# Kernel optimization log

Hardware: AMD Instinct MI355X
Metric: run time of the kernel (lower is better)

The kernel has to match this reference:

```python
import jax, jax.numpy as jnp
import numpy as np

E = 1024      # embed_dim
H = 16        # num_heads
D = E // H    # head_dim
F = 4096      # ff_dim
EPS = 1e-5


def setup_inputs() -> dict:
    key = jax.random.key(0)
    ks = jax.random.split(key, 12)
    s = 0.02
    return {
        "x": jax.random.normal(ks[0], (2, 2048, E), dtype=jnp.float32),
        "qkv_w": jax.random.normal(ks[1], (3 * E, E), dtype=jnp.float32) * s,
        "qkv_b": jnp.zeros((3 * E,), dtype=jnp.float32),
        "out_w": jax.random.normal(ks[2], (E, E), dtype=jnp.float32) * s,
        "out_b": jnp.zeros((E,), dtype=jnp.float32),
        "ff1_w": jax.random.normal(ks[3], (F, E), dtype=jnp.float32) * s,
        "ff1_b": jnp.zeros((F,), dtype=jnp.float32),
        "ff2_w": jax.random.normal(ks[4], (E, F), dtype=jnp.float32) * s,
        "ff2_b": jnp.zeros((E,), dtype=jnp.float32),
        "ln1_g": jnp.ones((E,), dtype=jnp.float32),
        "ln1_b": jnp.zeros((E,), dtype=jnp.float32),
        "ln2_g": jnp.ones((E,), dtype=jnp.float32),
        "ln2_b": jnp.zeros((E,), dtype=jnp.float32),
    }


def _layernorm(x, g, b):
    mu = jnp.mean(x, axis=-1, keepdims=True)
    var = jnp.mean(jnp.square(x - mu), axis=-1, keepdims=True)
    return (x - mu) * jax.lax.rsqrt(var + EPS) * g + b


def reference(x, qkv_w, qkv_b, out_w, out_b, ff1_w, ff1_b, ff2_w, ff2_b,
              ln1_g, ln1_b, ln2_g, ln2_b):
    B, S, _ = x.shape
    scale = D ** -0.5

    # --- attention sublayer (pre-LN) ---
    h = _layernorm(x, ln1_g, ln1_b)
    qkv = h @ qkv_w.T + qkv_b                          # [B,S,3E]
    qkv = qkv.reshape(B, S, 3, H, D)
    q, k, v = qkv[:, :, 0], qkv[:, :, 1], qkv[:, :, 2]  # [B,S,H,D]
    scores = jnp.einsum("bqhd,bkhd->bhqk", q, k) * scale
    attn = jax.nn.softmax(scores, axis=-1)
    o = jnp.einsum("bhqk,bkhd->bqhd", attn, v).reshape(B, S, E)
    x = x + o @ out_w.T + out_b

    # --- FFN sublayer (pre-LN, exact GELU) ---
    h = _layernorm(x, ln2_g, ln2_b)
    h = jax.nn.gelu(h @ ff1_w.T + ff1_b, approximate=False)
    x = x + h @ ff2_w.T + ff2_b
    return x
```

## Files before the change

### kernel.cpp

```cpp
#include <hip/hip_runtime.h>
#include <math.h>


typedef __attribute__((ext_vector_type(8))) short short8;
typedef __attribute__((ext_vector_type(4))) float f32x4;

__device__ __forceinline__ unsigned short f2bf(float f) {
  unsigned int u = __float_as_uint(f);
  u += 0x7fffu + ((u >> 16) & 1u);
  return (unsigned short)(u >> 16);
}

__device__ __forceinline__ float fexp2(float x) {
  return __builtin_amdgcn_exp2f(x);
}

__device__ __forceinline__ short8 pack8(float4 a, float4 b) {
  short8 p;
  p[0] = (short)f2bf(a.x); p[1] = (short)f2bf(a.y);
  p[2] = (short)f2bf(a.z); p[3] = (short)f2bf(a.w);
  p[4] = (short)f2bf(b.x); p[5] = (short)f2bf(b.y);
  p[6] = (short)f2bf(b.z); p[7] = (short)f2bf(b.w);
  return p;
}

__device__ __forceinline__ float gelu_fast(float v) {
  float g = 0.7978845608f * fmaf(0.044715f * v, v * v, v);
  float den = 1.0f + fexp2(-2.885390082f * g);
  return v * __builtin_amdgcn_rcpf(den);
}

__device__ __forceinline__ void async16(const void* g, void* l) {
  __builtin_amdgcn_global_load_lds(
      (const __attribute__((address_space(1))) unsigned int*)g,
      (__attribute__((address_space(3))) unsigned int*)l, 16, 0, 0);
}

__global__ __launch_bounds__(256) void conv_all(
    const float* __restrict__ i0, unsigned short* __restrict__ o0, int n0,
    const float* __restrict__ i1, unsigned short* __restrict__ o1, int n1,
    const float* __restrict__ i2, unsigned short* __restrict__ o2, int n2,
    const float* __restrict__ i3, unsigned short* __restrict__ o3, int n3) {
  int i = blockIdx.x * 256 + threadIdx.x;
  const float* in; unsigned short* out;
  if (i < n0) { in = i0; out = o0; }
  else if ((i -= n0) < n1) { in = i1; out = o1; }
  else if ((i -= n1) < n2) { in = i2; out = o2; }
  else { i -= n2; in = i3; out = o3; if (i >= n3) return; }
  float4 v = ((const float4*)in)[i];
  ushort4 u;
  u.x = f2bf(v.x); u.y = f2bf(v.y); u.z = f2bf(v.z); u.w = f2bf(v.w);
  ((ushort4*)out)[i] = u;
}

__global__ __launch_bounds__(256) void ln_kernel(const float* __restrict__ x,
                                                 const float* __restrict__ g,
                                                 const float* __restrict__ b,
                                                 unsigned short* __restrict__ out) {
  int row = blockIdx.x;
  int t = threadIdx.x;
  const float4* x4 = (const float4*)(x + (size_t)row * 1024);
  float4 v = x4[t];
  float s1 = v.x + v.y + v.z + v.w;
  float s2 = v.x * v.x + v.y * v.y + v.z * v.z + v.w * v.w;
  for (int off = 1; off < 64; off <<= 1) {
    s1 += __shfl_xor(s1, off, 64);
    s2 += __shfl_xor(s2, off, 64);
  }
  __shared__ float r1[4], r2[4];
  int w = t >> 6, lane = t & 63;
  if (lane == 0) { r1[w] = s1; r2[w] = s2; }
  __syncthreads();
  s1 = r1[0] + r1[1] + r1[2] + r1[3];
  s2 = r2[0] + r2[1] + r2[2] + r2[3];
  float mu = s1 * (1.0f / 1024.0f);
  float var = s2 * (1.0f / 1024.0f) - mu * mu;
  float rstd = rsqrtf(var + 1e-5f);
  int c = t * 4;
  float4 gv = ((const float4*)g)[t];
  float4 bv = ((const float4*)b)[t];
  unsigned short* o = out + (size_t)row * 1024 + c;
  o[0] = f2bf((v.x - mu) * rstd * gv.x + bv.x);
  o[1] = f2bf((v.y - mu) * rstd * gv.y + bv.y);
  o[2] = f2bf((v.z - mu) * rstd * gv.z + bv.z);
  o[3] = f2bf((v.w - mu) * rstd * gv.w + bv.w);
}

template <int MODE, int BM, int BN, int BK, int LIN, int NW, int WROWS>
__global__ __launch_bounds__(NW * 64) void gemm_bt(
    const unsigned short* __restrict__ A, const unsigned short* __restrict__ W,
    const float* __restrict__ bias, int M, int N, int K,
    const float* __restrict__ resid, float* __restrict__ out_f32,
    unsigned short* __restrict__ out_bf16,
    unsigned short* __restrict__ qbp, unsigned short* __restrict__ kbp,
    unsigned short* __restrict__ vtb) {
  constexpr int WCOLS = NW / WROWS;
  constexpr int WSPAN = BM / WROWS;
  constexpr int MI = WSPAN / 16;
  constexpr int CW = BN / WCOLS;
  constexpr int NJ = CW / 16;
  constexpr int LPR = BK / 8;
  constexpr int RPW = 512 / BK;
  constexpr int RRND = NW * RPW;
  constexpr int NIA = BM / RRND;
  constexpr int NIW = BN / RRND;
  constexpr int KK = BK / 32;
  static_assert(MODE != 0 || (NW == 4 && BN == 128 && WROWS == 2),
                "MODE 0 epilogue assumes NW=4/BN=128/WROWS=2");
  static_assert(MODE != 2 || CW == 64, "MODE 2 pack path assumes CW=64");
  __shared__ __attribute__((aligned(16))) unsigned short As[2][BM * BK];
  __shared__ __attribute__((aligned(16))) unsigned short Ws[2][BN * BK];
  int tid = threadIdx.x;
  int w = tid >> 6, lane = tid & 63, quad = lane >> 4, l16 = lane & 15;
  int wrow = w / WCOLS, wcol = w % WCOLS;
  int m0, n0;
  if (LIN) {
    int id = blockIdx.x;
    int mc = M / BM;
    m0 = (id % mc) * BM;
    n0 = (id / mc) * BN;
  } else {
    m0 = blockIdx.y * BM;
    n0 = blockIdx.x * BN;
  }

  int srow = lane / LPR;
  int sseg = lane % LPR;
  int ssw = (BK == 64) ? (srow & 7) : ((srow >> 1) & 3);
  int scol = (sseg ^ ssw) * 8;
  const unsigned short* Ag = A + (size_t)(m0 + w * RPW + srow) * K + scol;
  const unsigned short* Wg = W + (size_t)(n0 + w * RPW + srow) * K + scol;

  f32x4 acc[MI][NJ] = {};

#pragma unroll
  for (int i = 0; i < NIA; i++)
    async16(Ag + (size_t)(i * RRND) * K, As[0] + (i * RRND + w * RPW) * BK);
#pragma unroll
  for (int i = 0; i < NIW; i++)
    async16(Wg + (size_t)(i * RRND) * K, Ws[0] + (i * RRND + w * RPW) * BK);

  int fsw = (BK == 64) ? (l16 & 7) : ((l16 >> 1) & 3);

  for (int k0 = 0; k0 < K; k0 += BK) {
    int buf = (k0 / BK) & 1;
    __syncthreads();
    if (k0 + BK < K) {
      int nb = buf ^ 1;
#pragma unroll
      for (int i = 0; i < NIA; i++)
        async16(Ag + (size_t)(i * RRND) * K + k0 + BK, As[nb] + (i * RRND + w * RPW) * BK);
#pragma unroll
      for (int i = 0; i < NIW; i++)
        async16(Wg + (size_t)(i * RRND) * K + k0 + BK, Ws[nb] + (i * RRND + w * RPW) * BK);
    }
    if constexpr (MI >= 8) {
#pragma unroll
      for (int kk = 0; kk < KK; kk++) {
        short8 bfr[NJ];
#pragma unroll
        for (int j = 0; j < NJ; j++)
          bfr[j] = *(const short8*)(Ws[buf] + (wcol * CW + j * 16 + l16) * BK +
                                    ((kk * 4 + quad) ^ fsw) * 8);
#pragma unroll
        for (int i = 0; i < MI; i++) {
          short8 afr = *(const short8*)(As[buf] + (wrow * WSPAN + i * 16 + l16) * BK +
                                        ((kk * 4 + quad) ^ fsw) * 8);
#pragma unroll
          for (int j = 0; j < NJ; j++)
            acc[i][j] = __builtin_amdgcn_mfma_f32_16x16x32_bf16(afr, bfr[j], acc[i][j], 0, 0, 0);
        }
      }
    } else {
      short8 af[MI][KK], bf[NJ][KK];
#pragma unroll
      for (int i = 0; i < MI; i++)
#pragma unroll
        for (int kk = 0; kk < KK; kk++)
          af[i][kk] = *(const short8*)(As[buf] + (wrow * WSPAN + i * 16 + l16) * BK +
                                       ((kk * 4 + quad) ^ fsw) * 8);
#pragma unroll
      for (int j = 0; j < NJ; j++)
#pragma unroll
        for (int kk = 0; kk < KK; kk++)
          bf[j][kk] = *(const short8*)(Ws[buf] + (wcol * CW + j * 16 + l16) * BK +
                                       ((kk * 4 + quad) ^ fsw) * 8);
#pragma unroll
      for (int kk = 0; kk < KK; kk++)
#pragma unroll
        for (int i = 0; i < MI; i++)
#pragma unroll
          for (int j = 0; j < NJ; j++)
            acc[i][j] = __builtin_amdgcn_mfma_f32_16x16x32_bf16(af[i][kk], bf[j][kk], acc[i][j], 0, 0, 0);
    }
  }

  __syncthreads();
  constexpr int EPF = 16 * CW;
  float* ep = (w < NW / 2) ? ((float*)As + w * EPF)
                           : ((float*)Ws + (w - NW / 2) * EPF);
  int orow = lane >> 2;
  int oseg = lane & 3;
  int colbase = n0 + wcol * CW;
  float bv[NJ];
#pragma unroll
  for (int j = 0; j < NJ; j++) bv[j] = bias[colbase + j * 16 + l16];

  if (MODE == 1 || MODE == 2) {
#pragma unroll
    for (int i = 0; i < MI; i++) {
#pragma unroll
      for (int j = 0; j < NJ; j++)
#pragma unroll
        for (int r = 0; r < 4; r++) {
          int row = quad * 4 + r, col = j * 16 + l16;
          float v = acc[i][j][r] + bv[j];
          if (MODE == 2) v = gelu_fast(v);
          ep[row * CW + (((col >> 2) ^ (row & 7)) << 2) + (col & 3)] = v;
        }
      asm volatile("s_waitcnt lgkmcnt(0)" ::: "memory");
      int grow = m0 + wrow * WSPAN + i * 16 + orow;
      if (MODE == 1) {
#pragma unroll
        for (int t = 0; t < CW / 16; t++) {
          int sl = t * 4 + oseg;
          float4 v = *(float4*)(ep + orow * CW + ((sl ^ (orow & 7)) << 2));
          const float4 rv = *(const float4*)(resid + (size_t)grow * N + colbase + sl * 4);
          v.x += rv.x; v.y += rv.y; v.z += rv.z; v.w += rv.w;
          *(float4*)(out_f32 + (size_t)grow * N + colbase + sl * 4) = v;
        }
      } else {
#pragma unroll
        for (int t = 0; t < 2; t++) {
          int s0 = t * 8 + oseg * 2;
          float4 a = *(float4*)(ep + orow * 64 + ((s0 ^ (orow & 7)) << 2));
          float4 b = *(float4*)(ep + orow * 64 + (((s0 + 1) ^ (orow & 7)) << 2));
          *(short8*)(out_bf16 + (size_t)grow * N + colbase + t * 32 + oseg * 8) = pack8(a, b);
        }
      }
      asm volatile("s_waitcnt lgkmcnt(0)" ::: "memory");
    }
  } else {
    int whichW = colbase >> 10;
    int hh = (colbase & 1023) >> 6;
    int bh = (m0 >> 11) * 16 + hh;
    int sbase = (m0 & 2047) + wrow * WSPAN;
    if (whichW < 2) {
      unsigned short* dst0 = (whichW == 0) ? qbp : kbp;
      float qs = (whichW == 0) ? 0.1803368801f : 1.0f;
#pragma unroll
      for (int i = 0; i < MI; i++) {
#pragma unroll
        for (int j = 0; j < NJ; j++)
#pragma unroll
          for (int r = 0; r < 4; r++) {
            int row = quad * 4 + r, col = j * 16 + l16;
            ep[row * 64 + (((col >> 2) ^ (row & 7)) << 2) + (col & 3)] =
                (acc[i][j][r] + bv[j]) * qs;
          }
        asm volatile("s_waitcnt lgkmcnt(0)" ::: "memory");
        int s = sbase + i * 16 + orow;
#pragma unroll
        for (int t = 0; t < 2; t++) {
          int s0 = t * 8 + oseg * 2;
          float4 a = *(float4*)(ep + orow * 64 + ((s0 ^ (orow & 7)) << 2));
          float4 b = *(float4*)(ep + orow * 64 + (((s0 + 1) ^ (orow & 7)) << 2));
          *(short8*)(dst0 + ((size_t)bh * 2048 + s) * 64 + t * 32 + oseg * 8) = pack8(a, b);
        }
        asm volatile("s_waitcnt lgkmcnt(0)" ::: "memory");
      }
    } else {
#pragma unroll
      for (int j = 0; j < NJ; j++) {
#pragma unroll
        for (int i = 0; i < MI; i++) {
          float4 v4;
          v4.x = acc[i][j][0] + bv[j];
          v4.y = acc[i][j][1] + bv[j];
          v4.z = acc[i][j][2] + bv[j];
          v4.w = acc[i][j][3] + bv[j];
          *(float4*)(ep + l16 * 64 + (((i * 4 + quad) ^ (l16 & 7)) << 2)) = v4;
        }
        asm volatile("s_waitcnt lgkmcnt(0)" ::: "memory");
        int d = j * 16 + orow;
#pragma unroll
        for (int t = 0; t < 2; t++) {
          int s0 = t * 8 + oseg * 2;
          float4 a = *(float4*)(ep + orow * 64 + ((s0 ^ (orow & 7)) << 2));
          float4 b = *(float4*)(ep + orow * 64 + (((s0 + 1) ^ (orow & 7)) << 2));
          *(short8*)(vtb + ((size_t)bh * 64 + d) * 2048 + sbase + t * 32 + oseg * 8) = pack8(a, b);
        }
        asm volatile("s_waitcnt lgkmcnt(0)" ::: "memory");
      }
    }
  }
}

#define ALDP 72

__global__ __launch_bounds__(512) void attn_kernel(const unsigned short* __restrict__ qb,
                                                   const unsigned short* __restrict__ kb,
                                                   const unsigned short* __restrict__ vtb,
                                                   unsigned short* __restrict__ ob) {
  __shared__ __attribute__((aligned(16))) unsigned short Ks[2][64 * 64];
  __shared__ __attribute__((aligned(16))) unsigned short Vs[2][64 * 64];
  __shared__ __attribute__((aligned(16))) unsigned short Ps[8][16 * ALDP];

  int tid = threadIdx.x;
  int w = tid >> 6, lane = tid & 63, quad = lane >> 4, l16 = lane & 15;
  int bi = blockIdx.x;
  int bh = (bi & 7) * 4 + ((bi >> 3) & 3);
  int q0 = (bi >> 5) * 128 + w * 16;

  const unsigned short* qbase = qb + ((size_t)bh * 2048 + q0) * 64;
  const unsigned short* kbase = kb + (size_t)bh * 2048 * 64;
  const unsigned short* vbase = vtb + (size_t)bh * 64 * 2048;
  unsigned short* Pw = Ps[w];

  int srow = lane >> 3;
  int scol = ((lane & 7) ^ srow) * 8;
  const unsigned short* kg0 = kbase + (size_t)(w * 8 + srow) * 64 + scol;
  const unsigned short* vg0 = vbase + (size_t)(w * 8 + srow) * 2048 + scol;

  short8 qf[2];
  qf[0] = *(const short8*)(qbase + l16 * 64 + quad * 8);
  qf[1] = *(const short8*)(qbase + l16 * 64 + 32 + quad * 8);

  float lsum = 0.0f;
  f32x4 oacc[4] = {};
  int sw = l16 & 7;

  async16(kg0, &Ks[0][(w * 8) * 64]);
  async16(vg0, &Vs[0][(w * 8) * 64]);

  for (int c0 = 0; c0 < 2048; c0 += 64) {
    int buf = (c0 >> 6) & 1;
    __syncthreads();
    if (c0 + 64 < 2048) {
      int nb = buf ^ 1;
      async16(kg0 + (size_t)(c0 + 64) * 64, &Ks[nb][(w * 8) * 64]);
      async16(vg0 + c0 + 64, &Vs[nb][(w * 8) * 64]);
    }
    short8 kf[4][2];
#pragma unroll
    for (int t = 0; t < 4; t++) {
      const unsigned short* kr = &Ks[buf][(t * 16 + l16) * 64];
      kf[t][0] = *(const short8*)(kr + (quad ^ sw) * 8);
      kf[t][1] = *(const short8*)(kr + ((4 + quad) ^ sw) * 8);
    }
    f32x4 s[4];
#pragma unroll
    for (int t = 0; t < 4; t++) {
      f32x4 z = {0.0f, 0.0f, 0.0f, 0.0f};
      z = __builtin_amdgcn_mfma_f32_16x16x32_bf16(kf[t][0], qf[0], z, 0, 0, 0);
      z = __builtin_amdgcn_mfma_f32_16x16x32_bf16(kf[t][1], qf[1], z, 0, 0, 0);
      s[t] = z;
    }
    float rsum = 0.0f;
    unsigned short* pr = Pw + l16 * ALDP;
#pragma unroll
    for (int t = 0; t < 4; t++) {
      float p0 = fexp2(s[t][0]);
      float p1 = fexp2(s[t][1]);
      float p2 = fexp2(s[t][2]);
      float p3 = fexp2(s[t][3]);
      rsum += (p0 + p1) + (p2 + p3);
      uint2 pk;
      pk.x = __builtin_amdgcn_perm(__float_as_uint(p1), __float_as_uint(p0), 0x07060302u);
      pk.y = __builtin_amdgcn_perm(__float_as_uint(p3), __float_as_uint(p2), 0x07060302u);
      *(uint2*)(pr + t * 16 + quad * 4) = pk;
    }
    rsum += __shfl_xor(rsum, 16, 64);
    rsum += __shfl_xor(rsum, 32, 64);
    lsum += rsum;
    asm volatile("s_waitcnt lgkmcnt(0)" ::: "memory");
#pragma unroll
    for (int ks = 0; ks < 2; ks++) {
      short8 af = *(const short8*)(Pw + l16 * ALDP + ks * 32 + quad * 8);
#pragma unroll
      for (int j = 0; j < 4; j++) {
        short8 vf = *(const short8*)(&Vs[buf][(j * 16 + l16) * 64] +
                                     ((ks * 4 + quad) ^ sw) * 8);
        oacc[j] = __builtin_amdgcn_mfma_f32_16x16x32_bf16(af, vf, oacc[j], 0, 0, 0);
      }
    }
  }

  float linv[4];
#pragma unroll
  for (int r = 0; r < 4; r++)
    linv[r] = __builtin_amdgcn_rcpf(__shfl(lsum, quad * 4 + r, 64));
  int bb = bh >> 4, hh = bh & 15;
#pragma unroll
  for (int j = 0; j < 4; j++)
#pragma unroll
    for (int r = 0; r < 4; r++) {
      size_t tok = (size_t)bb * 2048 + q0 + quad * 4 + r;
      ob[tok * 1024 + hh * 64 + j * 16 + l16] = f2bf(oacc[j][r] * linv[r]);
    }
}

extern "C" void kernel_launch(void* const* d_in, const int* in_sizes, int n_in,
                              void* d_out, int out_size, void* d_ws, size_t ws_size,
                              hipStream_t stream) {
  (void)in_sizes; (void)n_in; (void)out_size; (void)ws_size;
  const float* x     = (const float*)d_in[0];
  const float* qkv_w = (const float*)d_in[1];
  const float* qkv_b = (const float*)d_in[2];
  const float* out_w = (const float*)d_in[3];
  const float* out_b = (const float*)d_in[4];
  const float* ff1_w = (const float*)d_in[5];
  const float* ff1_b = (const float*)d_in[6];
  const float* ff2_w = (const float*)d_in[7];
  const float* ff2_b = (const float*)d_in[8];
  const float* ln1_g = (const float*)d_in[9];
  const float* ln1_b = (const float*)d_in[10];
  const float* ln2_g = (const float*)d_in[11];
  const float* ln2_b = (const float*)d_in[12];
  float* out = (float*)d_out;
  char* ws = (char*)d_ws;

  const int M = 4096;

  unsigned short* WQ = (unsigned short*)(ws + 0);
  unsigned short* WO = (unsigned short*)(ws + 6291456);
  unsigned short* W1 = (unsigned short*)(ws + 8388608);
  unsigned short* W2 = (unsigned short*)(ws + 16777216);
  unsigned short* Hb = (unsigned short*)(ws + 25165824);
  unsigned short* Qb = (unsigned short*)(ws + 33554432);
  unsigned short* Kb = (unsigned short*)(ws + 41943040);
  unsigned short* VT = (unsigned short*)(ws + 50331648);
  unsigned short* Ob = (unsigned short*)(ws + 58720256);
  float*          X1 = (float*)(ws + 67108864);
  unsigned short* Gb = (unsigned short*)(ws + 33554432);

  conv_all<<<12288, 256, 0, stream>>>(qkv_w, WQ, 786432, out_w, WO, 262144,
                                      ff1_w, W1, 1048576, ff2_w, W2, 1048576);

  ln_kernel<<<4096, 256, 0, stream>>>(x, ln1_g, ln1_b, Hb);

  gemm_bt<0, 128, 128, 32, 0, 4, 2><<<dim3(24, 32), 256, 0, stream>>>(
      Hb, WQ, qkv_b, M, 3072, 1024, nullptr, nullptr, nullptr, Qb, Kb, VT);

  attn_kernel<<<512, 512, 0, stream>>>(Qb, Kb, VT, Ob);

  gemm_bt<1, 64, 128, 64, 1, 8, 2><<<512, 512, 0, stream>>>(
      Ob, WO, out_b, M, 1024, 1024, x, X1, nullptr, nullptr, nullptr, nullptr);

  ln_kernel<<<4096, 256, 0, stream>>>(X1, ln2_g, ln2_b, Hb);

  gemm_bt<2, 256, 256, 64, 0, 8, 2><<<dim3(16, 16), 512, 0, stream>>>(
      Hb, W1, ff1_b, M, 4096, 1024, nullptr, nullptr, Gb, nullptr, nullptr, nullptr);

  gemm_bt<1, 64, 128, 64, 1, 8, 2><<<512, 512, 0, stream>>>(
      Gb, W2, ff2_b, M, 1024, 4096, X1, out, nullptr, nullptr, nullptr, nullptr);
}
```

Before: 333.0 us.

## Process two query tiles per wave in attention to reuse K/V fragments

```diff
diff --git a/kernel.cpp b/kernel.cpp
--- a/kernel.cpp
+++ b/kernel.cpp
@@ -298,19 +298,19 @@
 
 #define ALDP 72
 
-__global__ __launch_bounds__(512) void attn_kernel(const unsigned short* __restrict__ qb,
+__global__ __launch_bounds__(256) void attn_kernel(const unsigned short* __restrict__ qb,
                                                    const unsigned short* __restrict__ kb,
                                                    const unsigned short* __restrict__ vtb,
                                                    unsigned short* __restrict__ ob) {
   __shared__ __attribute__((aligned(16))) unsigned short Ks[2][64 * 64];
   __shared__ __attribute__((aligned(16))) unsigned short Vs[2][64 * 64];
-  __shared__ __attribute__((aligned(16))) unsigned short Ps[8][16 * ALDP];
+  __shared__ __attribute__((aligned(16))) unsigned short Ps[4][2 * 16 * ALDP];
 
   int tid = threadIdx.x;
   int w = tid >> 6, lane = tid & 63, quad = lane >> 4, l16 = lane & 15;
   int bi = blockIdx.x;
   int bh = (bi & 7) * 4 + ((bi >> 3) & 3);
-  int q0 = (bi >> 5) * 128 + w * 16;
+  int q0 = (bi >> 5) * 128 + w * 32;
 
   const unsigned short* qbase = qb + ((size_t)bh * 2048 + q0) * 64;
   const unsigned short* kbase = kb + (size_t)bh * 2048 * 64;
@@ -319,27 +319,36 @@
 
   int srow = lane >> 3;
   int scol = ((lane & 7) ^ srow) * 8;
-  const unsigned short* kg0 = kbase + (size_t)(w * 8 + srow) * 64 + scol;
-  const unsigned short* vg0 = vbase + (size_t)(w * 8 + srow) * 2048 + scol;
-
-  short8 qf[2];
-  qf[0] = *(const short8*)(qbase + l16 * 64 + quad * 8);
-  qf[1] = *(const short8*)(qbase + l16 * 64 + 32 + quad * 8);
-
-  float lsum = 0.0f;
-  f32x4 oacc[4] = {};
+  const unsigned short* kg0 = kbase + (size_t)(w * 16 + srow) * 64 + scol;
+  const unsigned short* kg1 = kbase + (size_t)(w * 16 + 8 + srow) * 64 + scol;
+  const unsigned short* vg0 = vbase + (size_t)(w * 16 + srow) * 2048 + scol;
+  const unsigned short* vg1 = vbase + (size_t)(w * 16 + 8 + srow) * 2048 + scol;
+
+  short8 qf[2][2];
+#pragma unroll
+  for (int u = 0; u < 2; u++) {
+    qf[u][0] = *(const short8*)(qbase + (u * 16 + l16) * 64 + quad * 8);
+    qf[u][1] = *(const short8*)(qbase + (u * 16 + l16) * 64 + 32 + quad * 8);
+  }
+
+  float l0 = 0.0f, l1 = 0.0f;
+  f32x4 oacc[2][4] = {};
   int sw = l16 & 7;
 
-  async16(kg0, &Ks[0][(w * 8) * 64]);
-  async16(vg0, &Vs[0][(w * 8) * 64]);
+  async16(kg0, &Ks[0][(w * 16) * 64]);
+  async16(kg1, &Ks[0][(w * 16 + 8) * 64]);
+  async16(vg0, &Vs[0][(w * 16) * 64]);
+  async16(vg1, &Vs[0][(w * 16 + 8) * 64]);
 
   for (int c0 = 0; c0 < 2048; c0 += 64) {
     int buf = (c0 >> 6) & 1;
     __syncthreads();
     if (c0 + 64 < 2048) {
       int nb = buf ^ 1;
-      async16(kg0 + (size_t)(c0 + 64) * 64, &Ks[nb][(w * 8) * 64]);
-      async16(vg0 + c0 + 64, &Vs[nb][(w * 8) * 64]);
+      async16(kg0 + (size_t)(c0 + 64) * 64, &Ks[nb][(w * 16) * 64]);
+      async16(kg1 + (size_t)(c0 + 64) * 64, &Ks[nb][(w * 16 + 8) * 64]);
+      async16(vg0 + c0 + 64, &Vs[nb][(w * 16) * 64]);
+      async16(vg1 + c0 + 64, &Vs[nb][(w * 16 + 8) * 64]);
     }
     short8 kf[4][2];
 #pragma unroll
@@ -348,56 +357,69 @@
       kf[t][0] = *(const short8*)(kr + (quad ^ sw) * 8);
       kf[t][1] = *(const short8*)(kr + ((4 + quad) ^ sw) * 8);
     }
-    f32x4 s[4];
-#pragma unroll
-    for (int t = 0; t < 4; t++) {
-      f32x4 z = {0.0f, 0.0f, 0.0f, 0.0f};
-      z = __builtin_amdgcn_mfma_f32_16x16x32_bf16(kf[t][0], qf[0], z, 0, 0, 0);
-      z = __builtin_amdgcn_mfma_f32_16x16x32_bf16(kf[t][1], qf[1], z, 0, 0, 0);
-      s[t] = z;
-    }
-    float rsum = 0.0f;
-    unsigned short* pr = Pw + l16 * ALDP;
-#pragma unroll
-    for (int t = 0; t < 4; t++) {
-      float p0 = fexp2(s[t][0]);
-      float p1 = fexp2(s[t][1]);
-      float p2 = fexp2(s[t][2]);
-      float p3 = fexp2(s[t][3]);
-      rsum += (p0 + p1) + (p2 + p3);
-      uint2 pk;
-      pk.x = __builtin_amdgcn_perm(__float_as_uint(p1), __float_as_uint(p0), 0x07060302u);
-      pk.y = __builtin_amdgcn_perm(__float_as_uint(p3), __float_as_uint(p2), 0x07060302u);
-      *(uint2*)(pr + t * 16 + quad * 4) = pk;
-    }
-    rsum += __shfl_xor(rsum, 16, 64);
-    rsum += __shfl_xor(rsum, 32, 64);
-    lsum += rsum;
+    f32x4 s[2][4];
+#pragma unroll
+    for (int u = 0; u < 2; u++)
+#pragma unroll
+      for (int t = 0; t < 4; t++) {
+        f32x4 z = {0.0f, 0.0f, 0.0f, 0.0f};
+        z = __builtin_amdgcn_mfma_f32_16x16x32_bf16(kf[t][0], qf[u][0], z, 0, 0, 0);
+        z = __builtin_amdgcn_mfma_f32_16x16x32_bf16(kf[t][1], qf[u][1], z, 0, 0, 0);
+        s[u][t] = z;
+      }
+#pragma unroll
+    for (int u = 0; u < 2; u++) {
+      float rsum = 0.0f;
+      unsigned short* pr = Pw + (u * 16 + l16) * ALDP;
+#pragma unroll
+      for (int t = 0; t < 4; t++) {
+        float p0 = fexp2(s[u][t][0]);
+        float p1 = fexp2(s[u][t][1]);
+        float p2 = fexp2(s[u][t][2]);
+        float p3 = fexp2(s[u][t][3]);
+        rsum += (p0 + p1) + (p2 + p3);
+        uint2 pk;
+        pk.x = __builtin_amdgcn_perm(__float_as_uint(p1), __float_as_uint(p0), 0x07060302u);
+        pk.y = __builtin_amdgcn_perm(__float_as_uint(p3), __float_as_uint(p2), 0x07060302u);
+        *(uint2*)(pr + t * 16 + quad * 4) = pk;
+      }
+      rsum += __shfl_xor(rsum, 16, 64);
+      rsum += __shfl_xor(rsum, 32, 64);
+      if (u == 0) l0 += rsum; else l1 += rsum;
+    }
     asm volatile("s_waitcnt lgkmcnt(0)" ::: "memory");
 #pragma unroll
     for (int ks = 0; ks < 2; ks++) {
-      short8 af = *(const short8*)(Pw + l16 * ALDP + ks * 32 + quad * 8);
+      short8 af0 = *(const short8*)(Pw + l16 * ALDP + ks * 32 + quad * 8);
+      short8 af1 = *(const short8*)(Pw + (16 + l16) * ALDP + ks * 32 + quad * 8);
 #pragma unroll
       for (int j = 0; j < 4; j++) {
         short8 vf = *(const short8*)(&Vs[buf][(j * 16 + l16) * 64] +
                                      ((ks * 4 + quad) ^ sw) * 8);
-        oacc[j] = __builtin_amdgcn_mfma_f32_16x16x32_bf16(af, vf, oacc[j], 0, 0, 0);
-      }
-    }
-  }
-
-  float linv[4];
-#pragma unroll
-  for (int r = 0; r < 4; r++)
-    linv[r] = __builtin_amdgcn_rcpf(__shfl(lsum, quad * 4 + r, 64));
+        oacc[0][j] = __builtin_amdgcn_mfma_f32_16x16x32_bf16(af0, vf, oacc[0][j], 0, 0, 0);
+        oacc[1][j] = __builtin_amdgcn_mfma_f32_16x16x32_bf16(af1, vf, oacc[1][j], 0, 0, 0);
+      }
+    }
+  }
+
+  float linv[2][4];
+#pragma unroll
+  for (int u = 0; u < 2; u++) {
+    float lr = (u == 0) ? l0 : l1;
+#pragma unroll
+    for (int r = 0; r < 4; r++)
+      linv[u][r] = __builtin_amdgcn_rcpf(__shfl(lr, quad * 4 + r, 64));
+  }
   int bb = bh >> 4, hh = bh & 15;
 #pragma unroll
-  for (int j = 0; j < 4; j++)
-#pragma unroll
-    for (int r = 0; r < 4; r++) {
-      size_t tok = (size_t)bb * 2048 + q0 + quad * 4 + r;
-      ob[tok * 1024 + hh * 64 + j * 16 + l16] = f2bf(oacc[j][r] * linv[r]);
-    }
+  for (int u = 0; u < 2; u++)
+#pragma unroll
+    for (int j = 0; j < 4; j++)
+#pragma unroll
+      for (int r = 0; r < 4; r++) {
+        size_t tok = (size_t)bb * 2048 + q0 + u * 16 + quad * 4 + r;
+        ob[tok * 1024 + hh * 64 + j * 16 + l16] = f2bf(oacc[u][j][r] * linv[u][r]);
+      }
 }
 
 extern "C" void kernel_launch(void* const* d_in, const int* in_sizes, int n_in,
@@ -442,7 +464,7 @@
   gemm_bt<0, 128, 128, 32, 0, 4, 2><<<dim3(24, 32), 256, 0, stream>>>(
       Hb, WQ, qkv_b, M, 3072, 1024, nullptr, nullptr, nullptr, Qb, Kb, VT);
 
-  attn_kernel<<<512, 512, 0, stream>>>(Qb, Kb, VT, Ob);
+  attn_kernel<<<512, 256, 0, stream>>>(Qb, Kb, VT, Ob);
 
   gemm_bt<1, 64, 128, 64, 1, 8, 2><<<512, 512, 0, stream>>>(
       Ob, WO, out_b, M, 1024, 1024, x, X1, nullptr, nullptr, nullptr, nullptr);
```

Measured after the change: 336.1 us. About the same (+0.9%).
